# Performance work log

Measured on AMD Instinct MI355X. Metric: run time of the kernel, lower is better.

The kernel has to match this reference:

```python
import jax, jax.numpy as jnp
import numpy as np

STRIDES = (2, 2, 1)   # module init arg: (2,2,1) per docstring example
EPS = 1e-5            # InstanceNorm epsilon
ALPHA = 0.2           # leaky relu slope
DN = ('NDHWC', 'DHWIO', 'NDHWC')


def setup_inputs() -> dict:
    key = jax.random.key(0)
    k1, k2 = jax.random.split(key, 2)
    # x: [B, D, H, W, Cin] NDHWC volume batch
    x = jax.random.normal(k1, (4, 128, 128, 32, 32), dtype=jnp.float32)
    # w: per-sample hypernetwork kernels [B, kD, kH, kW, Cin, Cout]
    w = jax.random.normal(k2, (4, 3, 3, 3, 32, 64), dtype=jnp.float32) * 0.05
    # InstanceNorm affine params (learned)
    gamma = jnp.ones((64,), dtype=jnp.float32)
    beta = jnp.zeros((64,), dtype=jnp.float32)
    return {"x": x, "w": w, "gamma": gamma, "beta": beta}


def _per_sample_conv(xi, wi):
    # xi: [D,H,W,Cin], wi: [kD,kH,kW,Cin,Cout] -> [D',H',W',Cout]
    return jax.lax.conv_general_dilated(
        xi[None], wi, window_strides=STRIDES, padding='SAME',
        dimension_numbers=DN)[0]


def reference(x, w, gamma, beta):
    # batched dynamic conv: distinct kernel per sample, vectorized via vmap
    y = jax.vmap(_per_sample_conv)(x, w)          # [B, D', H', W', Cout]
    # InstanceNorm: normalize over spatial dims per sample, per channel
    mu = jnp.mean(y, axis=(1, 2, 3), keepdims=True)
    var = jnp.var(y, axis=(1, 2, 3), keepdims=True)
    y = (y - mu) * jax.lax.rsqrt(var + EPS) * gamma + beta
    # leaky relu alpha=0.2
    return jnp.where(y >= 0, y, ALPHA * y)
```

## Files before the change

### kernel.cpp

```cpp
#include <hip/hip_runtime.h>
#include <hip/hip_bf16.h>

#define B_ 4
#define D_ 128
#define H_ 128
#define W_ 32
#define CI 32
#define CO 64
#define OD 64
#define OH 64
#define OW 32
#define S_SPATIAL (OD*OH*OW)
#define EPS 1e-5f
#define ALPHA 0.2f

#define XROWS 9
#define ROWF 1024
#define SLICEF (XROWS*ROWF)
#define PLANEF (H_*ROWF)

typedef __attribute__((ext_vector_type(8))) short short8;
typedef __attribute__((ext_vector_type(4))) float f32x4;
typedef __attribute__((ext_vector_type(4))) unsigned u32x4;

__device__ inline short f2bf(float f) {
    return __builtin_bit_cast(short, __float2bfloat16(f));
}

__device__ inline short8 pack8(float4 a, float4 b) {
    short8 r;
    r[0]=f2bf(a.x); r[1]=f2bf(a.y); r[2]=f2bf(a.z); r[3]=f2bf(a.w);
    r[4]=f2bf(b.x); r[5]=f2bf(b.y); r[6]=f2bf(b.z); r[7]=f2bf(b.w);
    return r;
}

__device__ inline short8 mask_frag(short8 v, unsigned m) {
    u32x4 u = __builtin_bit_cast(u32x4, v);
    u[0]&=m; u[1]&=m; u[2]&=m; u[3]&=m;
    return __builtin_bit_cast(short8, u);
}

__device__ inline void gload16(const float* g, const float* l) {
    __builtin_amdgcn_global_load_lds(
        (const __attribute__((address_space(1))) void*)g,
        (__attribute__((address_space(3))) void*)l, 16, 0, 0);
}

__global__ __launch_bounds__(512) void zero_ws_kernel(float* ws) {
    ws[threadIdx.x] = 0.f;
}

__global__ __launch_bounds__(64) void wprep_kernel(const float* __restrict__ w,
                                                   short* __restrict__ wp) {
    int blk = blockIdx.x;
    int nf  = blk & 3;
    int tb  = blk >> 2;
    int l   = threadIdx.x;
    int l15 = l & 15, lhi = l >> 4;
    const float* wsrc = w + (size_t)tb * (CI*CO);
    short8 v;
#pragma unroll
    for (int j = 0; j < 8; ++j)
        v[j] = f2bf(wsrc[(lhi*8 + j)*CO + nf*16 + l15]);
    *(short8*)(wp + (size_t)blk*512 + l*8) = v;
}

__global__ __launch_bounds__(256, 2) void conv_mfma_kernel(const float* __restrict__ x,
                                                           const short* __restrict__ wp,
                                                           float* __restrict__ out,
                                                           float* __restrict__ ws) {
    const int bid = blockIdx.x;
    const int b   = bid >> 10;
    const int od  = (bid >> 4) & 63;
    const int oh0 = (bid & 15) << 2;
    const int t   = threadIdx.x;
    const int wv  = t >> 6;
    const int l   = t & 63;
    const int l15 = l & 15;
    const int lhi = l >> 4;

    const float* xb  = x + (size_t)b * (D_*PLANEF);
    const short* wpb = wp + (size_t)b * (27*2048);

    __shared__ __align__(16) float xbuf[2][SLICEF];
    __shared__ float lsum[4][64];
    __shared__ float lsq[4][64];

    const int lnF = (l << 2) ^ ((l & 0x38) >> 1);
    const int oh02 = oh0 * 2;

    auto stage = [&](const float* xsl, const float* buf) {
#pragma unroll
        for (int j = 0; j < 9; ++j) {
            int s = wv*9 + j;
            int r = s >> 2, q = s & 3;
            int ih = oh02 + r; if (ih > H_-1) ih = H_-1;
            gload16(xsl + (size_t)ih*ROWF + q*256 + lnF, buf + r*ROWF + q*256);
        }
    };

    f32x4 acc[2][4];
#pragma unroll
    for (int mf = 0; mf < 2; ++mf)
#pragma unroll
        for (int nf = 0; nf < 4; ++nf)
            acc[mf][nf] = (f32x4){0.f, 0.f, 0.f, 0.f};

    const unsigned mlo = (l15 == 0)  ? 0u : 0xFFFFFFFFu;
    const unsigned mhi = (l15 == 15) ? 0u : 0xFFFFFFFFu;
    const int ohw2 = 2*(oh0 + wv);

    auto compute = [&](int kd, const float* buf) {
        const short* wkd = wpb + (size_t)kd*(9*2048) + l*8;
#pragma unroll
        for (int kh = 0; kh < 3; ++kh) {
            short8 bf[3][4];
#pragma unroll
            for (int kw = 0; kw < 3; ++kw)
#pragma unroll
                for (int nf = 0; nf < 4; ++nf)
                    bf[kw][nf] = *(const short8*)(wkd + (kh*3 + kw)*2048 + nf*512);
            if (ohw2 + kh < H_) {
                const float* pr = buf + (2*wv + kh)*ROWF;
#pragma unroll
                for (int kw = 0; kw < 3; ++kw) {
#pragma unroll
                    for (int mf = 0; mf < 2; ++mf) {
                        int iw = mf*16 + l15 + kw - 1;
                        iw = iw < 0 ? 0 : (iw > 31 ? 31 : iw);
                        int o  = iw*32 + lhi*8;
                        int x4 = (iw & 7) << 2;
                        float4 v0 = *(const float4*)(pr + (o ^ x4));
                        float4 v1 = *(const float4*)(pr + ((o + 4) ^ x4));
                        short8 a = pack8(v0, v1);
                        if (kw == 0 && mf == 0) a = mask_frag(a, mlo);
                        if (kw == 2 && mf == 1) a = mask_frag(a, mhi);
                        acc[mf][0] = __builtin_amdgcn_mfma_f32_16x16x32_bf16(a, bf[kw][0], acc[mf][0], 0,0,0);
                        acc[mf][1] = __builtin_amdgcn_mfma_f32_16x16x32_bf16(a, bf[kw][1], acc[mf][1], 0,0,0);
                        acc[mf][2] = __builtin_amdgcn_mfma_f32_16x16x32_bf16(a, bf[kw][2], acc[mf][2], 0,0,0);
                        acc[mf][3] = __builtin_amdgcn_mfma_f32_16x16x32_bf16(a, bf[kw][3], acc[mf][3], 0,0,0);
                    }
                }
            }
        }
    };

    const int id0 = od*2;
    const float* xsl0 = xb + (size_t)id0 * PLANEF;
    const float* xsl1 = xsl0 + PLANEF;
    int id2c = id0 + 2; if (id2c > D_-1) id2c = D_-1;
    const float* xsl2 = xb + (size_t)id2c * PLANEF;

    stage(xsl0, xbuf[0]);
    stage(xsl1, xbuf[1]);
    asm volatile("s_waitcnt vmcnt(9)" ::: "memory");
    __builtin_amdgcn_s_barrier();
    __builtin_amdgcn_sched_barrier(0);
    compute(0, xbuf[0]);
    __builtin_amdgcn_s_barrier();
    __builtin_amdgcn_sched_barrier(0);
    stage(xsl2, xbuf[0]);
    asm volatile("s_waitcnt vmcnt(9)" ::: "memory");
    __builtin_amdgcn_s_barrier();
    __builtin_amdgcn_sched_barrier(0);
    compute(1, xbuf[1]);
    asm volatile("s_waitcnt vmcnt(0)" ::: "memory");
    __builtin_amdgcn_s_barrier();
    __builtin_amdgcn_sched_barrier(0);
    if (id0 + 2 < D_)
        compute(2, xbuf[0]);

    const int oh = oh0 + wv;
    float* yb = out + (size_t)((b*OD + od)*OH + oh) * (OW*CO);
#pragma unroll
    for (int mf = 0; mf < 2; ++mf)
#pragma unroll
        for (int nf = 0; nf < 4; ++nf)
#pragma unroll
            for (int r = 0; r < 4; ++r) {
                int ow = mf*16 + lhi*4 + r;
                int co = nf*16 + l15;
                yb[ow*CO + co] = acc[mf][nf][r];
            }

    float csum[4], csq[4];
#pragma unroll
    for (int nf = 0; nf < 4; ++nf) {
        float s = 0.f, q = 0.f;
#pragma unroll
        for (int mf = 0; mf < 2; ++mf)
#pragma unroll
            for (int r = 0; r < 4; ++r) {
                float v = acc[mf][nf][r];
                s += v;
                q = fmaf(v, v, q);
            }
        s += __shfl_xor(s, 16, 64); s += __shfl_xor(s, 32, 64);
        q += __shfl_xor(q, 16, 64); q += __shfl_xor(q, 32, 64);
        csum[nf] = s; csq[nf] = q;
    }
    if (lhi == 0) {
#pragma unroll
        for (int nf = 0; nf < 4; ++nf) {
            lsum[wv][nf*16 + l15] = csum[nf];
            lsq[wv][nf*16 + l15]  = csq[nf];
        }
    }
    __syncthreads();
    if (t < 64) {
        float s = lsum[0][t] + lsum[1][t] + lsum[2][t] + lsum[3][t];
        float q = lsq[0][t]  + lsq[1][t]  + lsq[2][t]  + lsq[3][t];
        atomicAdd(&ws[b*64 + t], s);
        atomicAdd(&ws[256 + b*64 + t], q);
    }
}

__global__ __launch_bounds__(256) void finalize_kernel(float* ws,
                                                       const float* __restrict__ gamma,
                                                       const float* __restrict__ beta) {
    int t = threadIdx.x;
    int co = t & 63;
    const float invS = 1.0f / (float)S_SPATIAL;
    float sum = ws[t];
    float sq  = ws[256 + t];
    float mu  = sum * invS;
    float var = sq * invS - mu*mu;
    float scale = rsqrtf(var + EPS) * gamma[co];
    ws[512 + t] = scale;
    ws[768 + t] = beta[co] - mu*scale;
}

__global__ __launch_bounds__(256) void norm_kernel(float* __restrict__ y,
                                                   const float* __restrict__ ws) {
    size_t i = (size_t)blockIdx.x * 256 + threadIdx.x;
    int b = (int)(i >> 21);
    const float4* scp = (const float4*)(ws + 512 + b*64);
    const float4* shp = (const float4*)(ws + 768 + b*64);
    float4 sc = scp[i & 15];
    float4 sh = shp[i & 15];
    float4 v = ((const float4*)y)[i];
    float4 r;
    r.x = fmaf(v.x, sc.x, sh.x);
    r.y = fmaf(v.y, sc.y, sh.y);
    r.z = fmaf(v.z, sc.z, sh.z);
    r.w = fmaf(v.w, sc.w, sh.w);
    r.x = r.x >= 0.f ? r.x : ALPHA * r.x;
    r.y = r.y >= 0.f ? r.y : ALPHA * r.y;
    r.z = r.z >= 0.f ? r.z : ALPHA * r.z;
    r.w = r.w >= 0.f ? r.w : ALPHA * r.w;
    ((float4*)y)[i] = r;
}

extern "C" void kernel_launch(void* const* d_in, const int* in_sizes, int n_in,
                              void* d_out, int out_size, void* d_ws, size_t ws_size,
                              hipStream_t stream) {
    const float* x     = (const float*)d_in[0];
    const float* w     = (const float*)d_in[1];
    const float* gamma = (const float*)d_in[2];
    const float* beta  = (const float*)d_in[3];
    float* out = (float*)d_out;
    float* ws  = (float*)d_ws;
    short* wp  = (short*)((char*)d_ws + 4096);

    zero_ws_kernel<<<1, 512, 0, stream>>>(ws);
    wprep_kernel<<<B_*27*4, 64, 0, stream>>>(w, wp);
    conv_mfma_kernel<<<B_*OD*(OH/4), 256, 0, stream>>>(x, wp, out, ws);
    finalize_kernel<<<1, 256, 0, stream>>>(ws, gamma, beta);
    norm_kernel<<<32768, 256, 0, stream>>>(out, ws);
}
```

Baseline: 216.6 us.

## Stage weights in LDS with double buffering and single-buffer the input slice

Weight fragments for each (kd,kh) chunk now arrive through direct global-to-LDS loads into a double buffer, replacing per-wave global loads of weights. The input slice buffer drops from two to one, which shrinks LDS per block. The schedule becomes nine steps, each with a full vmcnt(0) barrier, and the next plane loads only after the current one is consumed. This trades the earlier overlap of input plane loads with compute for fewer redundant global weight reads and lower LDS use, but adds more synchronisation points.

```diff
diff --git a/kernel.cpp b/kernel.cpp
--- a/kernel.cpp
+++ b/kernel.cpp
@@ -14,9 +14,9 @@
 #define EPS 1e-5f
 #define ALPHA 0.2f
 
-#define XROWS 9
 #define ROWF 1024
-#define SLICEF (XROWS*ROWF)
+#define XSLICEB (9*ROWF*4)
+#define WCHUNKB 12288
 #define PLANEF (H_*ROWF)
 
 typedef __attribute__((ext_vector_type(8))) short short8;
@@ -40,7 +40,7 @@
     return __builtin_bit_cast(short8, u);
 }
 
-__device__ inline void gload16(const float* g, const float* l) {
+__device__ inline void gload16(const void* g, const void* l) {
     __builtin_amdgcn_global_load_lds(
         (const __attribute__((address_space(1))) void*)g,
         (__attribute__((address_space(3))) void*)l, 16, 0, 0);
@@ -64,6 +64,15 @@
         v[j] = f2bf(wsrc[(lhi*8 + j)*CO + nf*16 + l15]);
     *(short8*)(wp + (size_t)blk*512 + l*8) = v;
 }
+
+#define VM0_BAR() \
+    asm volatile("s_waitcnt vmcnt(0) lgkmcnt(0)" ::: "memory"); \
+    __builtin_amdgcn_s_barrier(); \
+    __builtin_amdgcn_sched_barrier(0)
+
+#define BAR_ONLY() \
+    __builtin_amdgcn_s_barrier(); \
+    __builtin_amdgcn_sched_barrier(0)
 
 __global__ __launch_bounds__(256, 2) void conv_mfma_kernel(const float* __restrict__ x,
                                                            const short* __restrict__ wp,
@@ -82,21 +91,28 @@
     const float* xb  = x + (size_t)b * (D_*PLANEF);
     const short* wpb = wp + (size_t)b * (27*2048);
 
-    __shared__ __align__(16) float xbuf[2][SLICEF];
-    __shared__ float lsum[4][64];
-    __shared__ float lsq[4][64];
+    __shared__ __align__(16) char smem[XSLICEB + 2*WCHUNKB];
+    float* xbuf = (float*)smem;
+    char*  wbuf0 = smem + XSLICEB;
+    char*  wbuf1 = smem + XSLICEB + WCHUNKB;
 
     const int lnF = (l << 2) ^ ((l & 0x38) >> 1);
-    const int oh02 = oh0 * 2;
-
-    auto stage = [&](const float* xsl, const float* buf) {
-#pragma unroll
-        for (int j = 0; j < 9; ++j) {
-            int s = wv*9 + j;
-            int r = s >> 2, q = s & 3;
-            int ih = oh02 + r; if (ih > H_-1) ih = H_-1;
-            gload16(xsl + (size_t)ih*ROWF + q*256 + lnF, buf + r*ROWF + q*256);
-        }
+    const int seg = (t >> 6) & 3;
+
+    auto dma_x = [&](const float* plane) {
+#pragma unroll
+        for (int k = 0; k < 9; ++k) {
+            int ih = oh0*2 + k; if (ih > H_-1) ih = H_-1;
+            gload16(plane + (size_t)ih*ROWF + seg*256 + lnF,
+                    xbuf + k*ROWF + seg*256);
+        }
+    };
+    auto dma_w = [&](int chunk, char* wb) {
+        const short* src = wpb + (size_t)chunk*6144;
+#pragma unroll
+        for (int j = 0; j < 3; ++j)
+            gload16(src + j*2048 + (t >> 6)*512 + l*8,
+                    wb + j*4096 + (t >> 6)*1024);
     };
 
     f32x4 acc[2][4];
@@ -110,65 +126,62 @@
     const unsigned mhi = (l15 == 15) ? 0u : 0xFFFFFFFFu;
     const int ohw2 = 2*(oh0 + wv);
 
-    auto compute = [&](int kd, const float* buf) {
-        const short* wkd = wpb + (size_t)kd*(9*2048) + l*8;
+    auto compute3 = [&](int kh, const char* wb) {
+        const float* pr = xbuf + (2*wv + kh)*ROWF;
+#pragma unroll
+        for (int kw = 0; kw < 3; ++kw) {
+            const char* wpt = wb + kw*4096 + l*16;
+            short8 bf0 = *(const short8*)(wpt);
+            short8 bf1 = *(const short8*)(wpt + 1024);
+            short8 bf2 = *(const short8*)(wpt + 2048);
+            short8 bf3 = *(const short8*)(wpt + 3072);
+#pragma unroll
+            for (int mf = 0; mf < 2; ++mf) {
+                int iw = mf*16 + l15 + kw - 1;
+                iw = iw < 0 ? 0 : (iw > 31 ? 31 : iw);
+                int o  = iw*32 + lhi*8;
+                int x4 = (iw & 7) << 2;
+                float4 v0 = *(const float4*)(pr + (o ^ x4));
+                float4 v1 = *(const float4*)(pr + ((o + 4) ^ x4));
+                short8 a = pack8(v0, v1);
+                if (kw == 0 && mf == 0) a = mask_frag(a, mlo);
+                if (kw == 2 && mf == 1) a = mask_frag(a, mhi);
+                acc[mf][0] = __builtin_amdgcn_mfma_f32_16x16x32_bf16(a, bf0, acc[mf][0], 0,0,0);
+                acc[mf][1] = __builtin_amdgcn_mfma_f32_16x16x32_bf16(a, bf1, acc[mf][1], 0,0,0);
+                acc[mf][2] = __builtin_amdgcn_mfma_f32_16x16x32_bf16(a, bf2, acc[mf][2], 0,0,0);
+                acc[mf][3] = __builtin_amdgcn_mfma_f32_16x16x32_bf16(a, bf3, acc[mf][3], 0,0,0);
+            }
+        }
+    };
+
+    const int id0 = od*2;
+    const bool has2 = (id0 + 2) < D_;
+    const float* planes[3];
+    planes[0] = xb + (size_t)id0 * PLANEF;
+    planes[1] = planes[0] + PLANEF;
+    planes[2] = has2 ? (planes[1] + PLANEF) : planes[1];
+
+    dma_x(planes[0]);
+    dma_w(0, wbuf0);
+    VM0_BAR();
+
+    char* wb[2] = { wbuf0, wbuf1 };
+#pragma unroll
+    for (int kd = 0; kd < 3; ++kd) {
+        const bool kd_ok = (kd < 2) || has2;
 #pragma unroll
         for (int kh = 0; kh < 3; ++kh) {
-            short8 bf[3][4];
-#pragma unroll
-            for (int kw = 0; kw < 3; ++kw)
-#pragma unroll
-                for (int nf = 0; nf < 4; ++nf)
-                    bf[kw][nf] = *(const short8*)(wkd + (kh*3 + kw)*2048 + nf*512);
-            if (ohw2 + kh < H_) {
-                const float* pr = buf + (2*wv + kh)*ROWF;
-#pragma unroll
-                for (int kw = 0; kw < 3; ++kw) {
-#pragma unroll
-                    for (int mf = 0; mf < 2; ++mf) {
-                        int iw = mf*16 + l15 + kw - 1;
-                        iw = iw < 0 ? 0 : (iw > 31 ? 31 : iw);
-                        int o  = iw*32 + lhi*8;
-                        int x4 = (iw & 7) << 2;
-                        float4 v0 = *(const float4*)(pr + (o ^ x4));
-                        float4 v1 = *(const float4*)(pr + ((o + 4) ^ x4));
-                        short8 a = pack8(v0, v1);
-                        if (kw == 0 && mf == 0) a = mask_frag(a, mlo);
-                        if (kw == 2 && mf == 1) a = mask_frag(a, mhi);
-                        acc[mf][0] = __builtin_amdgcn_mfma_f32_16x16x32_bf16(a, bf[kw][0], acc[mf][0], 0,0,0);
-                        acc[mf][1] = __builtin_amdgcn_mfma_f32_16x16x32_bf16(a, bf[kw][1], acc[mf][1], 0,0,0);
-                        acc[mf][2] = __builtin_amdgcn_mfma_f32_16x16x32_bf16(a, bf[kw][2], acc[mf][2], 0,0,0);
-                        acc[mf][3] = __builtin_amdgcn_mfma_f32_16x16x32_bf16(a, bf[kw][3], acc[mf][3], 0,0,0);
-                    }
-                }
-            }
-        }
-    };
-
-    const int id0 = od*2;
-    const float* xsl0 = xb + (size_t)id0 * PLANEF;
-    const float* xsl1 = xsl0 + PLANEF;
-    int id2c = id0 + 2; if (id2c > D_-1) id2c = D_-1;
-    const float* xsl2 = xb + (size_t)id2c * PLANEF;
-
-    stage(xsl0, xbuf[0]);
-    stage(xsl1, xbuf[1]);
-    asm volatile("s_waitcnt vmcnt(9)" ::: "memory");
-    __builtin_amdgcn_s_barrier();
-    __builtin_amdgcn_sched_barrier(0);
-    compute(0, xbuf[0]);
-    __builtin_amdgcn_s_barrier();
-    __builtin_amdgcn_sched_barrier(0);
-    stage(xsl2, xbuf[0]);
-    asm volatile("s_waitcnt vmcnt(9)" ::: "memory");
-    __builtin_amdgcn_s_barrier();
-    __builtin_amdgcn_sched_barrier(0);
-    compute(1, xbuf[1]);
-    asm volatile("s_waitcnt vmcnt(0)" ::: "memory");
-    __builtin_amdgcn_s_barrier();
-    __builtin_amdgcn_sched_barrier(0);
-    if (id0 + 2 < D_)
-        compute(2, xbuf[0]);
+            const int c = kd*3 + kh;
+            if (c + 1 < 9) dma_w(c + 1, wb[(c + 1) & 1]);
+            if (kd_ok && (ohw2 + kh) < H_)
+                compute3(kh, wb[c & 1]);
+            if (kh == 2 && kd < 2) {
+                BAR_ONLY();
+                dma_x(planes[kd + 1]);
+            }
+            VM0_BAR();
+        }
+    }
 
     const int oh = oh0 + wv;
     float* yb = out + (size_t)((b*OD + od)*OH + oh) * (OW*CO);
@@ -183,6 +196,9 @@
                 yb[ow*CO + co] = acc[mf][nf][r];
             }
 
+    __syncthreads();
+    float* lsum = (float*)smem;
+    float* lsq  = (float*)(smem + 1024);
     float csum[4], csq[4];
 #pragma unroll
     for (int nf = 0; nf < 4; ++nf) {
@@ -202,14 +218,14 @@
     if (lhi == 0) {
 #pragma unroll
         for (int nf = 0; nf < 4; ++nf) {
-            lsum[wv][nf*16 + l15] = csum[nf];
-            lsq[wv][nf*16 + l15]  = csq[nf];
+            lsum[wv*64 + nf*16 + l15] = csum[nf];
+            lsq[wv*64 + nf*16 + l15]  = csq[nf];
         }
     }
     __syncthreads();
     if (t < 64) {
-        float s = lsum[0][t] + lsum[1][t] + lsum[2][t] + lsum[3][t];
-        float q = lsq[0][t]  + lsq[1][t]  + lsq[2][t]  + lsq[3][t];
+        float s = lsum[t] + lsum[64 + t] + lsum[128 + t] + lsum[192 + t];
+        float q = lsq[t]  + lsq[64 + t]  + lsq[128 + t]  + lsq[192 + t];
         atomicAdd(&ws[b*64 + t], s);
         atomicAdd(&ws[256 + b*64 + t], q);
     }
```

After: 244.5 us. 12.9% more time.
